# Performance work log

Hardware: AMD Instinct MI355X
Metric: run time of the kernel (lower is better)

Reference implementation:

```python
import jax, jax.numpy as jnp
import numpy as np

B, C, H, W = 2, 64, 128, 128
HEADS = 8
HID = C  # hidden_size = dim in MHSA.__init__
EPS = 1e-12  # F.normalize default eps


def setup_inputs() -> dict:
    key = jax.random.key(0)
    ks = jax.random.split(key, 9)
    s = 0.05
    return {
        "x": jax.random.normal(ks[0], (B, C, H, W), jnp.float32),
        "W1": jax.random.normal(ks[1], (C, HID), jnp.float32) * s,
        "b1": jax.random.normal(ks[2], (C, HID), jnp.float32) * s,
        "W2": jax.random.normal(ks[3], (C, HID, HID), jnp.float32) * s,
        "b2": jax.random.normal(ks[4], (C, HID), jnp.float32) * s,
        "W3": jax.random.normal(ks[5], (C, HID, 3), jnp.float32) * s,
        "b3": jax.random.normal(ks[6], (C, 3), jnp.float32) * s,
        "temperature": jnp.ones((HEADS, 1, 1), jnp.float32),
        "Wout": jax.random.normal(ks[7], (C, C), jnp.float32) * s,  # [out, in] 1x1 conv
        "bout": jax.random.normal(ks[8], (C,), jnp.float32) * s,
    }


def reference(x, W1, b1, W2, b2, W3, b3, temperature, Wout, bout):
    b, c, h, w = x.shape
    # KAN QKV projection: per-channel tiny MLPs, batched over the channel axis.
    xt = jnp.transpose(x, (0, 2, 3, 1)).reshape(-1, c)          # [N, C]
    h1 = jax.nn.relu(xt[:, :, None] * W1[None] + b1[None])      # [N, C, HID]
    h2 = jax.nn.relu(jnp.einsum('nch,chk->nck', h1, W2) + b2[None])  # [N, C, HID]
    o = jnp.einsum('nch,cho->nco', h2, W3) + b3[None]           # [N, C, 3]
    # torch.cat of per-channel 3-col outputs along dim=1 == reshape [N, C*3]
    qkv = o.reshape(b, h, w, c * 3)
    qkv = jnp.transpose(qkv, (0, 3, 1, 2))                      # [b, 3c, h, w]
    q, k, v = jnp.split(qkv, 3, axis=1)                         # each [b, c, h, w]

    def to_heads(t):
        return t.reshape(b, HEADS, c // HEADS, h * w)

    q, k, v = to_heads(q), to_heads(k), to_heads(v)
    # L2-normalize along the spatial (last) axis, torch F.normalize semantics
    q = q / jnp.maximum(jnp.linalg.norm(q, axis=-1, keepdims=True), EPS)
    k = k / jnp.maximum(jnp.linalg.norm(k, axis=-1, keepdims=True), EPS)
    # Channel attention: [b, head, c_h, c_h]
    attn = jnp.einsum('bhcn,bhdn->bhcd', q, k) * temperature[None]
    attn = jax.nn.softmax(attn, axis=-1)
    out = jnp.einsum('bhcd,bhdn->bhcn', attn, v)                # [b, head, c_h, hw]
    out = out.reshape(b, c, h, w)
    # 1x1 conv projection
    out = jnp.einsum('bchw,oc->bohw', out, Wout) + bout[None, :, None, None]
    return out
```

## Files before the change

kernel.cpp:

```cpp
#include <hip/hip_runtime.h>
#include <hip/hip_bf16.h>
#include <math.h>

#define HW 16384
#define NCH 64

#define NG   2048
#define X0   (-8.0f)
#define INVDX 128.0f
#define DX   0.0078125f
#define PSTR (64*2048)

typedef __attribute__((ext_vector_type(8))) short s16x8;
typedef __attribute__((ext_vector_type(4))) short s16x4;
typedef __attribute__((ext_vector_type(2))) float f32x2;
typedef __attribute__((ext_vector_type(4))) float f32x4;
typedef __attribute__((ext_vector_type(8))) float f32x8;
typedef __attribute__((ext_vector_type(2))) __bf16 bf16x2;
typedef __attribute__((ext_vector_type(8))) __bf16 bf16x8;
typedef __attribute__((ext_vector_type(4))) unsigned u32x4;
typedef __attribute__((ext_vector_type(2))) unsigned u32x2;

__device__ __forceinline__ short bf16b(float f) {
    union { __hip_bfloat16 h; short s; } u;
    u.h = __float2bfloat16(f);
    return u.s;
}
__device__ __forceinline__ s16x8 cvt8(f32x8 v) {
    return __builtin_bit_cast(s16x8, __builtin_convertvector(v, bf16x8));
}
__device__ __forceinline__ unsigned pk_h1(f32x2 xw, f32x2 w, f32x2 b, f32x2 z2) {
    const f32x2 h = __builtin_elementwise_max(__builtin_elementwise_fma(xw, w, b), z2);
    return __builtin_bit_cast(unsigned, __builtin_convertvector(h, bf16x2));
}
__device__ __forceinline__ unsigned pk_relu_cvt(f32x2 v, f32x2 z2) {
    const f32x2 g = __builtin_elementwise_max(v, z2);
    return __builtin_bit_cast(unsigned, __builtin_convertvector(g, bf16x2));
}

#if __has_builtin(__builtin_amdgcn_mfma_f32_16x16x16bf16_1k)
#define HAVE_MFMA16 1
#else
#define HAVE_MFMA16 0
#endif

__global__ __launch_bounds__(64, 4) void kan_grid_mfma(
    const float* __restrict__ W1,
    const float* __restrict__ b1,
    const float* __restrict__ W2,
    const float* __restrict__ b2,
    const float* __restrict__ W3,
    const float* __restrict__ b3,
    float* __restrict__ table)
{
    const int c     = blockIdx.x & 63;
    const int chunk = blockIdx.x >> 6;
    const int lane  = threadIdx.x;
    const int l15   = lane & 15;
    const int grp   = lane >> 4;

    __shared__ float W2s[4096];
    __shared__ float W1s[64], B1s[64], B2s[64];
    {
        const float4* src = (const float4*)(W2 + c * 4096);
        float4* dst = (float4*)W2s;
        for (int i = lane; i < 1024; i += 64) dst[i] = src[i];
        W1s[lane] = W1[c*64 + lane];
        B1s[lane] = b1[c*64 + lane];
        B2s[lane] = b2[c*64 + lane];
    }
    __syncthreads();

    const float* W3c = W3 + c * 192;

    s16x8 a1[4][2];
#pragma unroll
    for (int m = 0; m < 4; ++m)
#pragma unroll
        for (int s = 0; s < 2; ++s) {
            f32x8 w;
#pragma unroll
            for (int jj = 0; jj < 8; ++jj)
                w[jj] = W2s[(s*32 + grp*8 + jj)*64 + m*16 + l15];
            a1[m][s] = cvt8(w);
        }

#if HAVE_MFMA16
    s16x4 a2[4];
#pragma unroll
    for (int m = 0; m < 4; ++m) {
        s16x4 f;
#pragma unroll
        for (int jj = 0; jj < 4; ++jj) {
            const int k = m*16 + grp*4 + jj;
            f[jj] = (l15 < 3) ? bf16b(W3c[k*3 + l15]) : (short)0;
        }
        a2[m] = f;
    }
    f32x4 b3r;
#pragma unroll
    for (int r = 0; r < 4; ++r) {
        const int row = grp*4 + r;
        b3r[r] = (row < 3) ? b3[c*3 + row] : 0.f;
    }
#else
    const float b3v0 = b3[c*3+0], b3v1 = b3[c*3+1], b3v2 = b3[c*3+2];
#endif

    float* Tq = table + c*NG;
    const char* b2base = (const char*)B2s;
    const f32x2 z2 = {0.f, 0.f};

    for (int t = 0; t < 16; ++t) {
        int z;
        asm volatile("v_mov_b32 %0, 0" : "=v"(z));

        const int pt = chunk*256 + t*16 + l15;
        const float xv = X0 + (float)pt * DX;
        const f32x2 xw = {xv, xv};

        s16x8 bf[2];
#pragma unroll
        for (int s = 0; s < 2; ++s) {
            const f32x4 w1lo = *(const f32x4*)&W1s[z + s*32 + grp*8];
            const f32x4 w1hi = *(const f32x4*)&W1s[z + s*32 + grp*8 + 4];
            const f32x4 b1lo = *(const f32x4*)&B1s[z + s*32 + grp*8];
            const f32x4 b1hi = *(const f32x4*)&B1s[z + s*32 + grp*8 + 4];
            u32x4 p;
            p[0] = pk_h1(xw, (f32x2){w1lo[0], w1lo[1]}, (f32x2){b1lo[0], b1lo[1]}, z2);
            p[1] = pk_h1(xw, (f32x2){w1lo[2], w1lo[3]}, (f32x2){b1lo[2], b1lo[3]}, z2);
            p[2] = pk_h1(xw, (f32x2){w1hi[0], w1hi[1]}, (f32x2){b1hi[0], b1hi[1]}, z2);
            p[3] = pk_h1(xw, (f32x2){w1hi[2], w1hi[3]}, (f32x2){b1hi[2], b1hi[3]}, z2);
            bf[s] = __builtin_bit_cast(s16x8, p);
        }

        f32x4 acc[4];
#pragma unroll
        for (int m = 0; m < 4; ++m) {
            acc[m] = *(const f32x4*)(b2base + (m*64 + grp*16 + z));
            acc[m] = __builtin_amdgcn_mfma_f32_16x16x32_bf16(a1[m][0], bf[0], acc[m], 0, 0, 0);
            acc[m] = __builtin_amdgcn_mfma_f32_16x16x32_bf16(a1[m][1], bf[1], acc[m], 0, 0, 0);
        }

#if HAVE_MFMA16
        s16x4 bb[4];
#pragma unroll
        for (int m = 0; m < 4; ++m) {
            u32x2 pv;
            pv[0] = pk_relu_cvt((f32x2){acc[m][0], acc[m][1]}, z2);
            pv[1] = pk_relu_cvt((f32x2){acc[m][2], acc[m][3]}, z2);
            bb[m] = __builtin_bit_cast(s16x4, pv);
        }
        f32x4 acc2a = b3r;
        f32x4 acc2b = {0.f, 0.f, 0.f, 0.f};
        acc2a = __builtin_amdgcn_mfma_f32_16x16x16bf16_1k(a2[0], bb[0], acc2a, 0, 0, 0);
        acc2b = __builtin_amdgcn_mfma_f32_16x16x16bf16_1k(a2[1], bb[1], acc2b, 0, 0, 0);
        acc2a = __builtin_amdgcn_mfma_f32_16x16x16bf16_1k(a2[2], bb[2], acc2a, 0, 0, 0);
        acc2b = __builtin_amdgcn_mfma_f32_16x16x16bf16_1k(a2[3], bb[3], acc2b, 0, 0, 0);
        if (grp == 0) {
            Tq[pt]          = acc2a[0] + acc2b[0];
            Tq[PSTR + pt]   = acc2a[1] + acc2b[1];
            Tq[2*PSTR + pt] = acc2a[2] + acc2b[2];
        }
#else
        float po0 = 0.f, po1 = 0.f, po2 = 0.f;
#pragma unroll
        for (int m = 0; m < 4; ++m)
#pragma unroll
            for (int r = 0; r < 4; ++r) {
                const float g = fmaxf(acc[m][r], 0.f);
                const int k = m*16 + grp*4 + r;
                po0 = fmaf(g, W3c[k*3+0], po0);
                po1 = fmaf(g, W3c[k*3+1], po1);
                po2 = fmaf(g, W3c[k*3+2], po2);
            }
        po0 += __shfl_xor(po0, 16, 64); po0 += __shfl_xor(po0, 32, 64);
        po1 += __shfl_xor(po1, 16, 64); po1 += __shfl_xor(po1, 32, 64);
        po2 += __shfl_xor(po2, 16, 64); po2 += __shfl_xor(po2, 32, 64);
        if (grp == 0) {
            Tq[pt]          = po0 + b3v0;
            Tq[PSTR + pt]   = po1 + b3v1;
            Tq[2*PSTR + pt] = po2 + b3v2;
        }
#endif
    }
}

__global__ __launch_bounds__(256) void pwl_eval(
    const float* __restrict__ x, const float* __restrict__ table,
    float* __restrict__ qkv)
{
    const int c     = blockIdx.x >> 3;
    const int chunk = blockIdx.x & 7;
    const int t     = threadIdx.x;

    __shared__ float Lq[NG], Lk[NG], Lv[NG];
    const float4* Tq = (const float4*)(table + c*NG);
    const float4* Tk = (const float4*)(table + PSTR + c*NG);
    const float4* Tv = (const float4*)(table + 2*PSTR + c*NG);
    for (int i = t; i < NG/4; i += 256) {
        ((float4*)Lq)[i] = Tq[i];
        ((float4*)Lk)[i] = Tk[i];
        ((float4*)Lv)[i] = Tv[i];
    }
    __syncthreads();

    const int pxbase = chunk * 4096;
    const int b  = pxbase >> 14;
    const int hw = pxbase & 16383;
    const float* xr = x + (b*NCH + c)*HW + hw;
    float* q0 = qkv + (b*192 + c*3)*HW + hw;

    for (int i = 0; i < 16; ++i) {
        const int off = i*256 + t;
        const float xv = xr[off];
        const float u = (xv - X0) * INVDX;
        int idx = (int)u;
        idx = min(max(idx, 0), NG - 2);
        const float fr = u - (float)idx;
        const float q0v = Lq[idx], q1v = Lq[idx+1];
        const float k0v = Lk[idx], k1v = Lk[idx+1];
        const float v0v = Lv[idx], v1v = Lv[idx+1];
        q0[off]        = fmaf(fr, q1v - q0v, q0v);
        q0[HW + off]   = fmaf(fr, k1v - k0v, k0v);
        q0[2*HW + off] = fmaf(fr, v1v - v0v, v0v);
    }
}

__global__ __launch_bounds__(256) void dotpart_kernel(
    const float* __restrict__ qkv, float* __restrict__ dpart)
{
    const int bid = blockIdx.x;
    const int bhd = bid >> 4, spl = bid & 15;
    const int b = bhd >> 3, hd = bhd & 7;
    const int px = spl * 1024 + (int)threadIdx.x * 4;

    const float* qb = qkv + (b*192 + hd*8)*HW + px;
    float4 qv[8], kv[8];
#pragma unroll
    for (int r = 0; r < 8; ++r) qv[r] = *(const float4*)(qb + r*HW);
#pragma unroll
    for (int r = 0; r < 8; ++r) kv[r] = *(const float4*)(qb + (64+r)*HW);

    float acc[80];
#pragma unroll
    for (int p = 0; p < 80; ++p) acc[p] = 0.f;
#pragma unroll
    for (int e = 0; e < 4; ++e) {
        float qe[8], ke[8];
#pragma unroll
        for (int r = 0; r < 8; ++r) {
            qe[r] = ((const float*)&qv[r])[e];
            ke[r] = ((const float*)&kv[r])[e];
        }
#pragma unroll
        for (int i = 0; i < 8; ++i)
#pragma unroll
            for (int j = 0; j < 8; ++j)
                acc[i*8+j] = fmaf(qe[i], ke[j], acc[i*8+j]);
#pragma unroll
        for (int r = 0; r < 8; ++r) {
            acc[64+r] = fmaf(qe[r], qe[r], acc[64+r]);
            acc[72+r] = fmaf(ke[r], ke[r], acc[72+r]);
        }
    }
#pragma unroll
    for (int p = 0; p < 80; ++p) {
        float v = acc[p];
        for (int off = 1; off < 64; off <<= 1) v += __shfl_xor(v, off, 64);
        acc[p] = v;
    }
    __shared__ float red[4][80];
    const int wv = threadIdx.x >> 6, lane = threadIdx.x & 63;
    if (lane == 0) {
#pragma unroll
        for (int p = 0; p < 80; ++p) red[wv][p] = acc[p];
    }
    __syncthreads();
    const int t = threadIdx.x;
    if (t < 80)
        dpart[bid*80 + t] = red[0][t] + red[1][t] + red[2][t] + red[3][t];
}

__global__ __launch_bounds__(256) void out_kernel(
    const float* __restrict__ qkv, const float* __restrict__ dpart,
    const float* __restrict__ temp, const float* __restrict__ Wout,
    const float* __restrict__ bout, float* __restrict__ out)
{
    const int b    = blockIdx.x >> 8;
    const int qtr  = (blockIdx.x >> 6) & 3;
    const int tile = blockIdx.x & 63;
    const int n = tile * 256 + threadIdx.x;
    const int t = threadIdx.x;

    __shared__ float D[8][80];
    __shared__ float attnS[8][8][8];
    __shared__ float4 AtS[64][4];

    for (int idx = t; idx < 640; idx += 256) {
        const int g = idx / 80, p = idx % 80;
        float s = 0.f;
        for (int spl = 0; spl < 16; ++spl)
            s += dpart[((b*8 + g)*16 + spl)*80 + p];
        D[g][p] = s;
    }
    __syncthreads();

    if (t < 64) {
        const int hd = t >> 3, i = t & 7;
        const float invq = 1.f / fmaxf(sqrtf(D[hd][64+i]), 1e-12f);
        const float T = temp[hd];
        float l[8];
        float m = -1e30f;
#pragma unroll
        for (int j = 0; j < 8; ++j) {
            const float invk = 1.f / fmaxf(sqrtf(D[hd][72+j]), 1e-12f);
            l[j] = D[hd][i*8+j] * invq * invk * T;
            m = fmaxf(m, l[j]);
        }
        float s = 0.f;
#pragma unroll
        for (int j = 0; j < 8; ++j) { l[j] = expf(l[j] - m); s += l[j]; }
        const float inv = 1.f / s;
#pragma unroll
        for (int j = 0; j < 8; ++j) attnS[hd][i][j] = l[j] * inv;
    }
    __syncthreads();

    {
        const int cv = t & 63, oq = t >> 6;
        const int hd = cv >> 3, jj = cv & 7;
        float res[4];
#pragma unroll
        for (int oo = 0; oo < 4; ++oo) {
            const int o = qtr*16 + oq*4 + oo;
            float s = 0.f;
#pragma unroll
            for (int i = 0; i < 8; ++i)
                s = fmaf(Wout[o*64 + hd*8 + i], attnS[hd][i][jj], s);
            res[oo] = s;
        }
        AtS[cv][oq] = make_float4(res[0], res[1], res[2], res[3]);
    }
    __syncthreads();

    float acc[16];
#pragma unroll
    for (int o = 0; o < 16; ++o) acc[o] = 0.f;

    const float* vbase = qkv + (b*192 + 128)*HW + n;
    for (int cv = 0; cv < 64; ++cv) {
        const float vv = vbase[cv*HW];
#pragma unroll
        for (int o4 = 0; o4 < 4; ++o4) {
            const float4 w = AtS[cv][o4];
            acc[4*o4+0] = fmaf(w.x, vv, acc[4*o4+0]);
            acc[4*o4+1] = fmaf(w.y, vv, acc[4*o4+1]);
            acc[4*o4+2] = fmaf(w.z, vv, acc[4*o4+2]);
            acc[4*o4+3] = fmaf(w.w, vv, acc[4*o4+3]);
        }
    }
#pragma unroll
    for (int o = 0; o < 16; ++o) {
        const int oc = qtr*16 + o;
        out[(b*NCH + oc)*HW + n] = acc[o] + bout[oc];
    }
}

extern "C" void kernel_launch(void* const* d_in, const int* in_sizes, int n_in,
                              void* d_out, int out_size, void* d_ws, size_t ws_size,
                              hipStream_t stream) {
    const float* x    = (const float*)d_in[0];
    const float* W1   = (const float*)d_in[1];
    const float* b1   = (const float*)d_in[2];
    const float* W2   = (const float*)d_in[3];
    const float* b2   = (const float*)d_in[4];
    const float* W3   = (const float*)d_in[5];
    const float* b3   = (const float*)d_in[6];
    const float* temp = (const float*)d_in[7];
    const float* Wout = (const float*)d_in[8];
    const float* bout = (const float*)d_in[9];
    float* out = (float*)d_out;

    float* ws = (float*)d_ws;
    float* qkv   = ws;
    float* dpart = ws + 6291456;
    float* table = ws + 6291456 + 20480;

    kan_grid_mfma<<<512, 64, 0, stream>>>(W1, b1, W2, b2, W3, b3, table);
    pwl_eval<<<512, 256, 0, stream>>>(x, table, qkv);
    dotpart_kernel<<<256, 256, 0, stream>>>(qkv, dpart);
    out_kernel<<<512, 256, 0, stream>>>(qkv, dpart, temp, Wout, bout, out);
}
```

Measured before the change: 51.59 us.

## Fuse PWL evaluation into MFMA Gram kernel and store V as bf16

Q and K are no longer written to global memory. A new gram_kernel evaluates the piecewise-linear KAN table for the Q/K channels on the fly from bf16 tables in LDS and accumulates Q·K, Q·Q and K·K through bf16 MFMA. A separate v_eval kernel produces only the V channels, stored as bf16, and out_kernel reads that bf16 V. This removes a large fp32 qkv write and re-read. In exchange, the Gram entries and V carry bf16 rounding, and x is read twice.

```diff
diff --git a/kernel.cpp b/kernel.cpp
--- a/kernel.cpp
+++ b/kernel.cpp
@@ -25,6 +25,11 @@
     union { __hip_bfloat16 h; short s; } u;
     u.h = __float2bfloat16(f);
     return u.s;
+}
+__device__ __forceinline__ float bf2f(unsigned short us) {
+    union { unsigned u; float f; } x;
+    x.u = ((unsigned)us) << 16;
+    return x.f;
 }
 __device__ __forceinline__ s16x8 cvt8(f32x8 v) {
     return __builtin_bit_cast(s16x8, __builtin_convertvector(v, bf16x8));
@@ -186,104 +191,131 @@
     }
 }
 
-__global__ __launch_bounds__(256) void pwl_eval(
+__global__ __launch_bounds__(512) void gram_kernel(
     const float* __restrict__ x, const float* __restrict__ table,
-    float* __restrict__ qkv)
+    float* __restrict__ dpart)
 {
-    const int c     = blockIdx.x >> 3;
+    const int bhd = blockIdx.x >> 4;
+    const int spl = blockIdx.x & 15;
+    const int b = bhd >> 3, hd = bhd & 7;
+    const int tid = threadIdx.x;
+    const int w   = tid >> 6;
+    const int l   = tid & 63;
+    const int grp = l >> 4;
+    const int i16 = l & 15;
+    const int ch  = i16 & 7;
+    const int usek = i16 >> 3;
+
+    __shared__ unsigned short T[2][8][NG];
+
+    for (int e = tid; e < 8192; e += 512) {
+        const int map = e >> 12;
+        const int rem = e & 4095;
+        const int c8  = rem >> 9;
+        const int g   = rem & 511;
+        const int gm  = map*64 + hd*8 + c8;
+        const int cc  = gm / 3;
+        const int jj  = gm % 3;
+        const float4 v = ((const float4*)(table + jj*PSTR + cc*NG))[g];
+        u32x2 pk;
+        pk[0] = ((unsigned)(unsigned short)bf16b(v.x)) | (((unsigned)(unsigned short)bf16b(v.y)) << 16);
+        pk[1] = ((unsigned)(unsigned short)bf16b(v.z)) | (((unsigned)(unsigned short)bf16b(v.w)) << 16);
+        *(u32x2*)&T[map][c8][g*4] = pk;
+    }
+    __syncthreads();
+
+    const unsigned short* Tc = T[usek][ch];
+    const int gm = usek*64 + hd*8 + ch;
+    const int cx = gm / 3;
+    const float* xp = x + (b*NCH + cx)*HW + spl*1024 + grp*8;
+
+    f32x4 gacc = {0.f, 0.f, 0.f, 0.f};
+#pragma unroll
+    for (int s = 0; s < 4; ++s) {
+        const int slab = w*4 + s;
+        const float* xs = xp + slab*32;
+        const f32x4 xlo = *(const f32x4*)xs;
+        const f32x4 xhi = *(const f32x4*)(xs + 4);
+        f32x8 vals;
+#pragma unroll
+        for (int e = 0; e < 8; ++e) {
+            const float xv = (e < 4) ? xlo[e] : xhi[e-4];
+            const float u = (xv - X0) * INVDX;
+            int idx = (int)u;
+            idx = min(max(idx, 0), NG - 2);
+            const float fr = u - (float)idx;
+            const float t0 = bf2f(Tc[idx]);
+            const float t1 = bf2f(Tc[idx+1]);
+            vals[e] = fmaf(fr, t1 - t0, t0);
+        }
+        const s16x8 frag = cvt8(vals);
+        gacc = __builtin_amdgcn_mfma_f32_16x16x32_bf16(frag, frag, gacc, 0, 0, 0);
+    }
+
+    __syncthreads();
+    float* red = (float*)&T[0][0][0];
+#pragma unroll
+    for (int r = 0; r < 4; ++r)
+        red[w*256 + (grp*4 + r)*16 + i16] = gacc[r];
+    __syncthreads();
+
+    if (tid < 256) {
+        const int row = tid >> 4, col = tid & 15;
+        float g = 0.f;
+#pragma unroll
+        for (int ww = 0; ww < 8; ++ww) g += red[ww*256 + tid];
+        int p = -1;
+        if (row < 8 && col >= 8)      p = row*8 + (col - 8);
+        else if (row == col && row < 8) p = 64 + row;
+        else if (row == col)            p = 72 + (row - 8);
+        if (p >= 0) dpart[(bhd*16 + spl)*80 + p] = g;
+    }
+}
+
+__global__ __launch_bounds__(256) void v_eval(
+    const float* __restrict__ x, const float* __restrict__ table,
+    unsigned short* __restrict__ vbuf)
+{
+    const int m     = blockIdx.x >> 3;
     const int chunk = blockIdx.x & 7;
     const int t     = threadIdx.x;
-
-    __shared__ float Lq[NG], Lk[NG], Lv[NG];
-    const float4* Tq = (const float4*)(table + c*NG);
-    const float4* Tk = (const float4*)(table + PSTR + c*NG);
-    const float4* Tv = (const float4*)(table + 2*PSTR + c*NG);
-    for (int i = t; i < NG/4; i += 256) {
-        ((float4*)Lq)[i] = Tq[i];
-        ((float4*)Lk)[i] = Tk[i];
-        ((float4*)Lv)[i] = Tv[i];
-    }
+    const int gm    = 128 + m;
+    const int cx    = gm / 3;
+    const int jj    = gm % 3;
+
+    __shared__ float Lv[NG];
+    const float4* Tv = (const float4*)(table + jj*PSTR + cx*NG);
+    for (int i = t; i < NG/4; i += 256) ((float4*)Lv)[i] = Tv[i];
     __syncthreads();
 
     const int pxbase = chunk * 4096;
     const int b  = pxbase >> 14;
     const int hw = pxbase & 16383;
-    const float* xr = x + (b*NCH + c)*HW + hw;
-    float* q0 = qkv + (b*192 + c*3)*HW + hw;
-
-    for (int i = 0; i < 16; ++i) {
-        const int off = i*256 + t;
-        const float xv = xr[off];
-        const float u = (xv - X0) * INVDX;
-        int idx = (int)u;
-        idx = min(max(idx, 0), NG - 2);
-        const float fr = u - (float)idx;
-        const float q0v = Lq[idx], q1v = Lq[idx+1];
-        const float k0v = Lk[idx], k1v = Lk[idx+1];
-        const float v0v = Lv[idx], v1v = Lv[idx+1];
-        q0[off]        = fmaf(fr, q1v - q0v, q0v);
-        q0[HW + off]   = fmaf(fr, k1v - k0v, k0v);
-        q0[2*HW + off] = fmaf(fr, v1v - v0v, v0v);
-    }
-}
-
-__global__ __launch_bounds__(256) void dotpart_kernel(
-    const float* __restrict__ qkv, float* __restrict__ dpart)
-{
-    const int bid = blockIdx.x;
-    const int bhd = bid >> 4, spl = bid & 15;
-    const int b = bhd >> 3, hd = bhd & 7;
-    const int px = spl * 1024 + (int)threadIdx.x * 4;
-
-    const float* qb = qkv + (b*192 + hd*8)*HW + px;
-    float4 qv[8], kv[8];
-#pragma unroll
-    for (int r = 0; r < 8; ++r) qv[r] = *(const float4*)(qb + r*HW);
-#pragma unroll
-    for (int r = 0; r < 8; ++r) kv[r] = *(const float4*)(qb + (64+r)*HW);
-
-    float acc[80];
-#pragma unroll
-    for (int p = 0; p < 80; ++p) acc[p] = 0.f;
-#pragma unroll
-    for (int e = 0; e < 4; ++e) {
-        float qe[8], ke[8];
-#pragma unroll
-        for (int r = 0; r < 8; ++r) {
-            qe[r] = ((const float*)&qv[r])[e];
-            ke[r] = ((const float*)&kv[r])[e];
-        }
-#pragma unroll
-        for (int i = 0; i < 8; ++i)
-#pragma unroll
-            for (int j = 0; j < 8; ++j)
-                acc[i*8+j] = fmaf(qe[i], ke[j], acc[i*8+j]);
-#pragma unroll
-        for (int r = 0; r < 8; ++r) {
-            acc[64+r] = fmaf(qe[r], qe[r], acc[64+r]);
-            acc[72+r] = fmaf(ke[r], ke[r], acc[72+r]);
-        }
-    }
-#pragma unroll
-    for (int p = 0; p < 80; ++p) {
-        float v = acc[p];
-        for (int off = 1; off < 64; off <<= 1) v += __shfl_xor(v, off, 64);
-        acc[p] = v;
-    }
-    __shared__ float red[4][80];
-    const int wv = threadIdx.x >> 6, lane = threadIdx.x & 63;
-    if (lane == 0) {
-#pragma unroll
-        for (int p = 0; p < 80; ++p) red[wv][p] = acc[p];
-    }
-    __syncthreads();
-    const int t = threadIdx.x;
-    if (t < 80)
-        dpart[bid*80 + t] = red[0][t] + red[1][t] + red[2][t] + red[3][t];
+    const float* xr = x + (b*NCH + cx)*HW + hw;
+    unsigned short* vr = vbuf + (b*NCH + m)*HW + hw;
+
+    for (int i = 0; i < 8; ++i) {
+        const int off = i*512 + t*2;
+        const float2 xv = *(const float2*)(xr + off);
+        float o[2];
+#pragma unroll
+        for (int e = 0; e < 2; ++e) {
+            const float u = ((e ? xv.y : xv.x) - X0) * INVDX;
+            int idx = (int)u;
+            idx = min(max(idx, 0), NG - 2);
+            const float fr = u - (float)idx;
+            const float v0 = Lv[idx], v1 = Lv[idx+1];
+            o[e] = fmaf(fr, v1 - v0, v0);
+        }
+        ushort2 vs;
+        vs.x = (unsigned short)bf16b(o[0]);
+        vs.y = (unsigned short)bf16b(o[1]);
+        *(ushort2*)(vr + off) = vs;
+    }
 }
 
 __global__ __launch_bounds__(256) void out_kernel(
-    const float* __restrict__ qkv, const float* __restrict__ dpart,
+    const unsigned short* __restrict__ vbuf, const float* __restrict__ dpart,
     const float* __restrict__ temp, const float* __restrict__ Wout,
     const float* __restrict__ bout, float* __restrict__ out)
 {
@@ -348,9 +380,9 @@
 #pragma unroll
     for (int o = 0; o < 16; ++o) acc[o] = 0.f;
 
-    const float* vbase = qkv + (b*192 + 128)*HW + n;
+    const unsigned short* vbase = vbuf + (b*NCH)*HW + n;
     for (int cv = 0; cv < 64; ++cv) {
-        const float vv = vbase[cv*HW];
+        const float vv = bf2f(vbase[cv*HW]);
 #pragma unroll
         for (int o4 = 0; o4 < 4; ++o4) {
             const float4 w = AtS[cv][o4];
@@ -383,12 +415,12 @@
     float* out = (float*)d_out;
 
     float* ws = (float*)d_ws;
-    float* qkv   = ws;
-    float* dpart = ws + 6291456;
-    float* table = ws + 6291456 + 20480;
+    float* table = ws;
+    float* dpart = ws + 393216;
+    unsigned short* vbuf = (unsigned short*)(ws + 393216 + 20480);
 
     kan_grid_mfma<<<512, 64, 0, stream>>>(W1, b1, W2, b2, W3, b3, table);
-    pwl_eval<<<512, 256, 0, stream>>>(x, table, qkv);
-    dotpart_kernel<<<256, 256, 0, stream>>>(qkv, dpart);
-    out_kernel<<<512, 256, 0, stream>>>(qkv, dpart, temp, Wout, bout, out);
-}
+    gram_kernel<<<256, 512, 0, stream>>>(x, table, dpart);
+    v_eval<<<512, 256, 0, stream>>>(x, table, vbuf);
+    out_kernel<<<512, 256, 0, stream>>>(vbuf, dpart, temp, Wout, bout, out);
+}
```

New measurement: 52.78 us. 2.3% more time.
